# Performance work log

Measured on AMD Instinct MI355X. Metric: run time of the kernel, lower is better.

Reference implementation:

```python
import jax, jax.numpy as jnp
import numpy as np

FP8_MAX = 448.0  # finfo(float8_e4m3fn).max
G = 128          # quantization block size


def _fp8_roundtrip(x):
    # emulate storage/rounding in float8_e4m3fn
    return x.astype(jnp.float8_e4m3fn).astype(jnp.float32)


def _quant_dequant_act(x, g=G):
    """Dynamic per-token, per-128-column-group fp8 quantization, then dequant.
    Matches fp8_act_quant: scale = amax(group)/FP8_MAX, q = clip(x/scale)."""
    lead, K = x.shape[:-1], x.shape[-1]
    xg = x.reshape(*lead, K // g, g)
    amax = jnp.max(jnp.abs(xg), axis=-1, keepdims=True)
    scale = jnp.maximum(amax, 1e-10) / FP8_MAX
    q = _fp8_roundtrip(jnp.clip(xg / scale, -FP8_MAX, FP8_MAX))
    return (q * scale).reshape(*lead, K)


def _dequant_weight(w, s, g=G):
    """Block-wise dequant: w [E,O,K] fp8 codes (stored as f32), s [E,O/g,K/g] scales."""
    E, O, K = w.shape
    wb = w.reshape(E, O // g, g, K // g, g)
    return (wb * s[:, :, None, :, None]).reshape(E, O, K)


def setup_inputs() -> dict:
    key = jax.random.key(0)
    ks = jax.random.split(key, 7)
    T, H, I, E, TK = 2048, 1024, 512, 16, 4
    hidden_states = jax.random.normal(ks[0], (T, H), dtype=jnp.float32)
    top_k_index = jax.random.randint(ks[1], (T, TK), 0, E)
    top_k_weights = jax.nn.softmax(jax.random.normal(ks[2], (T, TK), dtype=jnp.float32), axis=-1)
    # fp8-representable weight codes + positive block scale grids
    gate_up_proj = _fp8_roundtrip(jax.random.normal(ks[3], (E, 2 * I, H), dtype=jnp.float32) * 8.0)
    gate_up_proj_scale_inv = jax.random.uniform(ks[4], (E, (2 * I) // G, H // G), dtype=jnp.float32,
                                                minval=0.001, maxval=0.005)
    down_proj = _fp8_roundtrip(jax.random.normal(ks[5], (E, H, I), dtype=jnp.float32) * 8.0)
    down_proj_scale_inv = jax.random.uniform(ks[6], (E, H // G, I // G), dtype=jnp.float32,
                                             minval=0.001, maxval=0.005)
    return {
        "hidden_states": hidden_states,
        "top_k_index": top_k_index,
        "top_k_weights": top_k_weights,
        "gate_up_proj": gate_up_proj,
        "gate_up_proj_scale_inv": gate_up_proj_scale_inv,
        "down_proj": down_proj,
        "down_proj_scale_inv": down_proj_scale_inv,
    }


def reference(hidden_states, top_k_index, top_k_weights,
              gate_up_proj, gate_up_proj_scale_inv,
              down_proj, down_proj_scale_inv):
    E = gate_up_proj.shape[0]
    # dynamic activation quant (identical for every expert, since tokens are just gathered rows)
    x_deq = _quant_dequant_act(hidden_states)                       # [T, H]
    w_gu = _dequant_weight(gate_up_proj, gate_up_proj_scale_inv)    # [E, 2I, H]
    w_dn = _dequant_weight(down_proj, down_proj_scale_inv)          # [E, H, I]
    # gate_up GEMM for all experts; tokens not routed to e contribute with weight 0 below
    gate_up = jnp.einsum('th,eoh->teo', x_deq, w_gu)                # [T, E, 2I]
    gate, up = jnp.split(gate_up, 2, axis=-1)
    h = jax.nn.silu(gate) * up                                      # [T, E, I]
    h_deq = _quant_dequant_act(h)                                   # re-quantize intermediate
    expert_out = jnp.einsum('tei,ehi->teh', h_deq, w_dn)            # [T, E, H]
    # routing weight per (token, expert): sum of top_k weights whose index == e
    rw = jnp.einsum('tk,tke->te', top_k_weights,
                    jax.nn.one_hot(top_k_index, E, dtype=hidden_states.dtype))
    return jnp.einsum('teh,te->th', expert_out, rw)                 # [T, H] float32 accumulation
```

## Files before the change

### kernel.cpp

```cpp
#include <hip/hip_runtime.h>
#include <math.h>

#define T_TOK 2048
#define H_DIM 1024
#define I_DIM 512
#define N_EXP 16
#define TOPK  4
#define NPAIR (T_TOK*TOPK)

typedef unsigned short u16;
typedef __attribute__((ext_vector_type(8))) short s8v;
typedef __attribute__((ext_vector_type(4))) float f4v;

#define GLDS(g, l) __builtin_amdgcn_global_load_lds( \
    (const __attribute__((address_space(1))) void*)(g), \
    (__attribute__((address_space(3))) void*)(l), 16, 0, 0)

__device__ __forceinline__ float fp8_rt(float v) {
    float av = fabsf(v);
    if (av < 0.015625f) {
        return rintf(v * 512.0f) * 0.001953125f;
    }
    unsigned u = __float_as_uint(v);
    unsigned lsb = (u >> 20) & 1u;
    u = (u + 0x7FFFFu + lsb) & 0xFFF00000u;
    return __uint_as_float(u);
}

__device__ __forceinline__ unsigned f2bf(float v) {
    return __float_as_uint(v) >> 16;
}

#define NF4_GU (N_EXP * 2 * I_DIM * H_DIM / 4)
__global__ void k_prep(const float* __restrict__ wgu, u16* __restrict__ wgu_bf,
                       const float* __restrict__ wdn, u16* __restrict__ wdn_bf,
                       const float* __restrict__ x, u16* __restrict__ xq,
                       float* __restrict__ xs, const int* __restrict__ tki,
                       int* __restrict__ counts, int* __restrict__ lists) {
    int bid = blockIdx.x, tid = threadIdx.x;
    if (bid < 24576) {
        int i = bid * 256 + tid;
        const float* in = wgu; u16* out = wgu_bf;
        if (i >= NF4_GU) { in = wdn; out = wdn_bf; i -= NF4_GU; }
        float4 a = ((const float4*)in)[i];
        int2 st;
        st.x = (int)(f2bf(a.x) | (f2bf(a.y) << 16));
        st.y = (int)(f2bf(a.z) | (f2bf(a.w) << 16));
        ((int2*)out)[i] = st;
    } else {
        int t = bid - 24576;
        if (tid < 4) {
            int p = t * 4 + tid;
            int e = tki[p];
            int pos = atomicAdd(&counts[e], 1);
            lists[e * NPAIR + pos] = p;
        }
        float4 v = ((const float4*)(x + (size_t)t * H_DIM))[tid];
        float a = fmaxf(fmaxf(fabsf(v.x), fabsf(v.y)), fmaxf(fabsf(v.z), fabsf(v.w)));
        #pragma unroll
        for (int m = 16; m >= 1; m >>= 1) a = fmaxf(a, __shfl_xor(a, m));
        float s = fmaxf(a, 1e-10f) / 448.0f;
        ushort4 r;
        r.x = (u16)f2bf(fp8_rt(fminf(fmaxf(v.x / s, -448.f), 448.f)));
        r.y = (u16)f2bf(fp8_rt(fminf(fmaxf(v.y / s, -448.f), 448.f)));
        r.z = (u16)f2bf(fp8_rt(fminf(fmaxf(v.z / s, -448.f), 448.f)));
        r.w = (u16)f2bf(fp8_rt(fminf(fmaxf(v.w / s, -448.f), 448.f)));
        ((ushort4*)(xq + (size_t)t * H_DIM))[tid] = r;
        if ((tid & 31) == 0) xs[t * 8 + (tid >> 5)] = s;
    }
}

__global__ __launch_bounds__(256, 3)
void k_gateup(const u16* __restrict__ xq, const float* __restrict__ xs,
              const int* __restrict__ counts, const int* __restrict__ lists,
              const u16* __restrict__ wgu, const float* __restrict__ sgu,
              const u16* __restrict__ zbuf, float* __restrict__ hbuf) {
    int bid = blockIdx.x;
    int e = bid & 15, tile = bid >> 4;
    int tt = tile >> 3, it = tile & 7;
    int n = counts[e];
    if (tt * 64 >= n) return;

    __shared__ __align__(16) u16 sm[2][12288];
    __shared__ float xs_l[64][8];
    __shared__ int ptok[64];

    int tid = threadIdx.x;
    int w = tid >> 6, lane = tid & 63;
    int m = w & 1, q = w >> 1;
    int l15 = lane & 15, l4 = lane >> 4;

    if (tid < 64) {
        int slot = tt * 64 + tid;
        ptok[tid] = (slot < n) ? lists[e * NPAIR + slot] : -1;
    }
    __syncthreads();
    {
        int r = tid >> 2, kb4 = (tid & 3) * 2;
        int p = ptok[r];
        xs_l[r][kb4]     = (p >= 0) ? xs[(p >> 2) * 8 + kb4]     : 0.f;
        xs_l[r][kb4 + 1] = (p >= 0) ? xs[(p >> 2) * 8 + kb4 + 1] : 0.f;
    }

    const u16* wbase = wgu + (size_t)e * 1024 * 1024;
    const u16* srcB[4];
    #pragma unroll
    for (int j = 0; j < 4; ++j) {
        int s = j * 256 + tid;
        int row = s >> 3, c = s & 7, cg = c ^ (row & 7);
        int nrow = (row < 64) ? it * 64 + row : 448 + it * 64 + row;
        srcB[j] = wbase + (size_t)nrow * H_DIM + cg * 8;
    }
    const u16* srcA[2];
    #pragma unroll
    for (int j = 0; j < 2; ++j) {
        int s = j * 256 + tid;
        int row = s >> 3, c = s & 7, cg = c ^ (row & 7);
        int p = ptok[row];
        srcA[j] = (p >= 0) ? xq + (size_t)(p >> 2) * H_DIM + cg * 8 : zbuf;
    }

    int idxA[2][2], idxB[4][2];
    #pragma unroll
    for (int fm = 0; fm < 2; ++fm) {
        int ar = m * 32 + fm * 16 + l15;
        #pragma unroll
        for (int kg = 0; kg < 2; ++kg)
            idxA[fm][kg] = 8192 + ar * 64 + (((kg * 4 + l4) ^ (ar & 7)) * 8);
    }
    #pragma unroll
    for (int nf = 0; nf < 4; ++nf) {
        int br = q * 64 + nf * 16 + l15;
        #pragma unroll
        for (int kg = 0; kg < 2; ++kg)
            idxB[nf][kg] = br * 64 + (((kg * 4 + l4) ^ (br & 7)) * 8);
    }

    auto stage = [&](int buf) {
        #pragma unroll
        for (int j = 0; j < 4; ++j) { GLDS(srcB[j], &sm[buf][j * 2048 + tid * 8]); srcB[j] += 64; }
        #pragma unroll
        for (int j = 0; j < 2; ++j) { GLDS(srcA[j], &sm[buf][8192 + j * 2048 + tid * 8]); srcA[j] += 64; }
    };

    f4v master[2][4], part[2][4];
    #pragma unroll
    for (int a = 0; a < 2; ++a)
        #pragma unroll
        for (int b = 0; b < 4; ++b) { master[a][b] = (f4v){0,0,0,0}; part[a][b] = (f4v){0,0,0,0}; }

    const float* swp = sgu + e * 64 + (q ? 4 + (it >> 1) : (it >> 1)) * 8;

    stage(0);
    __syncthreads();

    for (int t = 0; t < 16; ++t) {
        if (t < 15) stage((t + 1) & 1);
        const u16* buf = &sm[t & 1][0];
        #pragma unroll
        for (int kg = 0; kg < 2; ++kg) {
            s8v a0 = *(const s8v*)&buf[idxA[0][kg]];
            s8v a1 = *(const s8v*)&buf[idxA[1][kg]];
            #pragma unroll
            for (int nf = 0; nf < 4; ++nf) {
                s8v b = *(const s8v*)&buf[idxB[nf][kg]];
                part[0][nf] = __builtin_amdgcn_mfma_f32_16x16x32_bf16(a0, b, part[0][nf], 0, 0, 0);
                part[1][nf] = __builtin_amdgcn_mfma_f32_16x16x32_bf16(a1, b, part[1][nf], 0, 0, 0);
            }
        }
        if (t & 1) {
            int kb = t >> 1;
            float sw = swp[kb];
            #pragma unroll
            for (int fm = 0; fm < 2; ++fm) {
                float c0 = xs_l[m * 32 + fm * 16 + l4 * 4 + 0][kb] * sw;
                float c1 = xs_l[m * 32 + fm * 16 + l4 * 4 + 1][kb] * sw;
                float c2 = xs_l[m * 32 + fm * 16 + l4 * 4 + 2][kb] * sw;
                float c3 = xs_l[m * 32 + fm * 16 + l4 * 4 + 3][kb] * sw;
                #pragma unroll
                for (int nf = 0; nf < 4; ++nf) {
                    master[fm][nf][0] += c0 * part[fm][nf][0];
                    master[fm][nf][1] += c1 * part[fm][nf][1];
                    master[fm][nf][2] += c2 * part[fm][nf][2];
                    master[fm][nf][3] += c3 * part[fm][nf][3];
                    part[fm][nf] = (f4v){0,0,0,0};
                }
            }
        }
        __syncthreads();
    }

    float* Ul = (float*)sm;
    if (q == 1) {
        #pragma unroll
        for (int fm = 0; fm < 2; ++fm)
            #pragma unroll
            for (int nf = 0; nf < 4; ++nf)
                #pragma unroll
                for (int r = 0; r < 4; ++r)
                    Ul[(m * 32 + fm * 16 + l4 * 4 + r) * 65 + nf * 16 + l15] = master[fm][nf][r];
    }
    __syncthreads();
    if (q == 0) {
        #pragma unroll
        for (int fm = 0; fm < 2; ++fm)
            #pragma unroll
            for (int r = 0; r < 4; ++r) {
                int row = m * 32 + fm * 16 + l4 * 4 + r;
                int p = ptok[row];
                if (p < 0) continue;
                float* drow = hbuf + (size_t)p * I_DIM + it * 64;
                #pragma unroll
                for (int nf = 0; nf < 4; ++nf) {
                    float g = master[fm][nf][r];
                    float u = Ul[row * 65 + nf * 16 + l15];
                    drow[nf * 16 + l15] = (g / (1.0f + expf(-g))) * u;
                }
            }
    }
}

__global__ void k_quant_h(const float* __restrict__ h, u16* __restrict__ hq,
                          float* __restrict__ hs) {
    int p = blockIdx.x, tid = threadIdx.x;
    float4 v = ((const float4*)(h + (size_t)p * I_DIM))[tid];
    float a = fmaxf(fmaxf(fabsf(v.x), fabsf(v.y)), fmaxf(fabsf(v.z), fabsf(v.w)));
    #pragma unroll
    for (int m = 16; m >= 1; m >>= 1) a = fmaxf(a, __shfl_xor(a, m));
    float s = fmaxf(a, 1e-10f) / 448.0f;
    ushort4 r;
    r.x = (u16)f2bf(fp8_rt(fminf(fmaxf(v.x / s, -448.f), 448.f)));
    r.y = (u16)f2bf(fp8_rt(fminf(fmaxf(v.y / s, -448.f), 448.f)));
    r.z = (u16)f2bf(fp8_rt(fminf(fmaxf(v.z / s, -448.f), 448.f)));
    r.w = (u16)f2bf(fp8_rt(fminf(fmaxf(v.w / s, -448.f), 448.f)));
    ((ushort4*)(hq + (size_t)p * I_DIM))[tid] = r;
    if ((tid & 31) == 0) hs[p * 4 + (tid >> 5)] = s;
}

__global__ __launch_bounds__(256, 3)
void k_down(const u16* __restrict__ hq, const float* __restrict__ hs,
            const int* __restrict__ counts, const int* __restrict__ lists,
            const u16* __restrict__ wdn, const float* __restrict__ sdn,
            const float* __restrict__ tkw, const u16* __restrict__ zbuf,
            float* __restrict__ dout) {
    int bid = blockIdx.x;
    int e = bid & 15, tile = bid >> 4;
    int tt = tile >> 3, nt = tile & 7;
    int n = counts[e];
    if (tt * 64 >= n) return;

    __shared__ __align__(16) u16 sm[2][12288];
    __shared__ float hs_l[64][4];
    __shared__ float rw_l[64];
    __shared__ int ptok[64];

    int tid = threadIdx.x;
    int w = tid >> 6, lane = tid & 63;
    int m = w & 1, q = w >> 1;
    int l15 = lane & 15, l4 = lane >> 4;

    if (tid < 64) {
        int slot = tt * 64 + tid;
        ptok[tid] = (slot < n) ? lists[e * NPAIR + slot] : -1;
    }
    __syncthreads();
    {
        int r = tid >> 2, kb = tid & 3;
        int p = ptok[r];
        hs_l[r][kb] = (p >= 0) ? hs[p * 4 + kb] : 0.f;
        if (tid < 64) rw_l[tid] = (ptok[tid] >= 0) ? tkw[ptok[tid]] : 0.f;
    }

    const u16* wbase = wdn + (size_t)e * H_DIM * I_DIM;
    const u16* srcB[4];
    #pragma unroll
    for (int j = 0; j < 4; ++j) {
        int s = j * 256 + tid;
        int row = s >> 3, c = s & 7, cg = c ^ (row & 7);
        srcB[j] = wbase + (size_t)(nt * 128 + row) * I_DIM + cg * 8;
    }
    const u16* srcA[2];
    #pragma unroll
    for (int j = 0; j < 2; ++j) {
        int s = j * 256 + tid;
        int row = s >> 3, c = s & 7, cg = c ^ (row & 7);
        int p = ptok[row];
        srcA[j] = (p >= 0) ? hq + (size_t)p * I_DIM + cg * 8 : zbuf;
    }

    int idxA[2][2], idxB[4][2];
    #pragma unroll
    for (int fm = 0; fm < 2; ++fm) {
        int ar = m * 32 + fm * 16 + l15;
        #pragma unroll
        for (int kg = 0; kg < 2; ++kg)
            idxA[fm][kg] = 8192 + ar * 64 + (((kg * 4 + l4) ^ (ar & 7)) * 8);
    }
    #pragma unroll
    for (int nf = 0; nf < 4; ++nf) {
        int br = q * 64 + nf * 16 + l15;
        #pragma unroll
        for (int kg = 0; kg < 2; ++kg)
            idxB[nf][kg] = br * 64 + (((kg * 4 + l4) ^ (br & 7)) * 8);
    }

    auto stage = [&](int buf) {
        #pragma unroll
        for (int j = 0; j < 4; ++j) { GLDS(srcB[j], &sm[buf][j * 2048 + tid * 8]); srcB[j] += 64; }
        #pragma unroll
        for (int j = 0; j < 2; ++j) { GLDS(srcA[j], &sm[buf][8192 + j * 2048 + tid * 8]); srcA[j] += 64; }
    };

    f4v master[2][4], part[2][4];
    #pragma unroll
    for (int a = 0; a < 2; ++a)
        #pragma unroll
        for (int b = 0; b < 4; ++b) { master[a][b] = (f4v){0,0,0,0}; part[a][b] = (f4v){0,0,0,0}; }

    const float* swp = sdn + (e * 8 + nt) * 4;

    stage(0);
    __syncthreads();

    for (int t = 0; t < 8; ++t) {
        if (t < 7) stage((t + 1) & 1);
        const u16* buf = &sm[t & 1][0];
        #pragma unroll
        for (int kg = 0; kg < 2; ++kg) {
            s8v a0 = *(const s8v*)&buf[idxA[0][kg]];
            s8v a1 = *(const s8v*)&buf[idxA[1][kg]];
            #pragma unroll
            for (int nf = 0; nf < 4; ++nf) {
                s8v b = *(const s8v*)&buf[idxB[nf][kg]];
                part[0][nf] = __builtin_amdgcn_mfma_f32_16x16x32_bf16(a0, b, part[0][nf], 0, 0, 0);
                part[1][nf] = __builtin_amdgcn_mfma_f32_16x16x32_bf16(a1, b, part[1][nf], 0, 0, 0);
            }
        }
        if (t & 1) {
            int kb = t >> 1;
            float sw = swp[kb];
            #pragma unroll
            for (int fm = 0; fm < 2; ++fm) {
                float c0 = hs_l[m * 32 + fm * 16 + l4 * 4 + 0][kb] * sw;
                float c1 = hs_l[m * 32 + fm * 16 + l4 * 4 + 1][kb] * sw;
                float c2 = hs_l[m * 32 + fm * 16 + l4 * 4 + 2][kb] * sw;
                float c3 = hs_l[m * 32 + fm * 16 + l4 * 4 + 3][kb] * sw;
                #pragma unroll
                for (int nf = 0; nf < 4; ++nf) {
                    master[fm][nf][0] += c0 * part[fm][nf][0];
                    master[fm][nf][1] += c1 * part[fm][nf][1];
                    master[fm][nf][2] += c2 * part[fm][nf][2];
                    master[fm][nf][3] += c3 * part[fm][nf][3];
                    part[fm][nf] = (f4v){0,0,0,0};
                }
            }
        }
        __syncthreads();
    }

    #pragma unroll
    for (int fm = 0; fm < 2; ++fm)
        #pragma unroll
        for (int r = 0; r < 4; ++r) {
            int row = m * 32 + fm * 16 + l4 * 4 + r;
            int p = ptok[row];
            if (p < 0) continue;
            float rw = rw_l[row];
            float* drow = dout + (size_t)p * H_DIM + nt * 128 + q * 64;
            #pragma unroll
            for (int nf = 0; nf < 4; ++nf)
                drow[nf * 16 + l15] = rw * master[fm][nf][r];
        }
}

__global__ void k_reduce(const float* __restrict__ dout, float* __restrict__ out) {
    int i = blockIdx.x * 256 + threadIdx.x;
    int t = i >> 8, h4 = i & 255;
    const float4* d = (const float4*)dout;
    float4 a = d[(size_t)(t * 4 + 0) * 256 + h4];
    float4 b = d[(size_t)(t * 4 + 1) * 256 + h4];
    float4 c = d[(size_t)(t * 4 + 2) * 256 + h4];
    float4 e = d[(size_t)(t * 4 + 3) * 256 + h4];
    float4 r;
    r.x = a.x + b.x + c.x + e.x;
    r.y = a.y + b.y + c.y + e.y;
    r.z = a.z + b.z + c.z + e.z;
    r.w = a.w + b.w + c.w + e.w;
    ((float4*)out)[i] = r;
}

extern "C" void kernel_launch(void* const* d_in, const int* in_sizes, int n_in,
                              void* d_out, int out_size, void* d_ws, size_t ws_size,
                              hipStream_t stream) {
    const float* hs_in = (const float*)d_in[0];
    const int*   tki = (const int*)d_in[1];
    const float* tkw = (const float*)d_in[2];
    const float* wgu = (const float*)d_in[3];
    const float* sgu = (const float*)d_in[4];
    const float* wdn = (const float*)d_in[5];
    const float* sdn = (const float*)d_in[6];
    float* out = (float*)d_out;

    char* ws = (char*)d_ws;
    const size_t MB = 1024 * 1024;
    u16*   wgu_bf = (u16*)(ws);
    float* dout   = (float*)(ws);
    u16*   wdn_bf = (u16*)(ws + 32 * MB);
    u16*   xq     = (u16*)(ws + 48 * MB);
    float* xs     = (float*)(ws + 52 * MB);
    float* hbuf   = (float*)(ws + 53 * MB);
    u16*   hq     = (u16*)(ws + 69 * MB);
    float* hs     = (float*)(ws + 77 * MB);
    int*   counts = (int*)(ws + 78 * MB);
    u16*   zbuf   = (u16*)(ws + 78 * MB + 4096);
    int*   lists  = (int*)(ws + 78 * MB + 65536);

    hipMemsetAsync(ws + 78 * MB, 0, 8192, stream);

    k_prep<<<26624, 256, 0, stream>>>(wgu, wgu_bf, wdn, wdn_bf, hs_in, xq, xs,
                                      tki, counts, lists);
    k_gateup<<<2048, 256, 0, stream>>>(xq, xs, counts, lists, wgu_bf, sgu, zbuf, hbuf);
    k_quant_h<<<NPAIR, 128, 0, stream>>>(hbuf, hq, hs);
    k_down<<<2048, 256, 0, stream>>>(hq, hs, counts, lists, wdn_bf, sdn, tkw, zbuf, dout);
    k_reduce<<<T_TOK * H_DIM / 1024, 256, 0, stream>>>(dout, out);
}
```

Measured before the change: 249.6 us.

## Switch expert GEMMs from bf16 to native fp8 MFMA with byte-packed operands

Weights and quantized activations are now stored as packed fp8 e4m3 bytes instead of bf16, and both expert GEMMs use the fp8 MFMA instruction. This halves the bytes written by the prep kernel and the bytes streamed into LDS by the GEMMs, and halves the K-loop trip count since each 128-byte row holds a full 128-element scale block. The block scale is now applied every iteration instead of every other one. Routing is moved into a separate single-block kernel that counts with LDS atomics, which adds one launch and a serial 8192-pair pass. The handwritten fp8 encoder must match the hardware e4m3 format, including denormals.

```diff
diff --git a/kernel.cpp b/kernel.cpp
--- a/kernel.cpp
+++ b/kernel.cpp
@@ -9,7 +9,7 @@
 #define NPAIR (T_TOK*TOPK)
 
 typedef unsigned short u16;
-typedef __attribute__((ext_vector_type(8))) short s8v;
+typedef unsigned char u8;
 typedef __attribute__((ext_vector_type(4))) float f4v;
 
 #define GLDS(g, l) __builtin_amdgcn_global_load_lds( \
@@ -27,61 +27,73 @@
     return __uint_as_float(u);
 }
 
-__device__ __forceinline__ unsigned f2bf(float v) {
-    return __float_as_uint(v) >> 16;
+__device__ __forceinline__ unsigned f2fp8(float v) {
+    unsigned u = __float_as_uint(v);
+    unsigned s = (u >> 24) & 0x80u;
+    float av = fabsf(v);
+    if (av < 0.015625f) return s | (unsigned)(av * 512.0f);
+    unsigned e = ((u >> 23) & 0xFFu) - 120u;
+    return s | (e << 3) | ((u >> 20) & 7u);
+}
+
+__global__ void k_route2(const int* __restrict__ tki, int* __restrict__ counts,
+                         int* __restrict__ lists) {
+    __shared__ int cnt[16];
+    int tid = threadIdx.x;
+    if (tid < 16) cnt[tid] = 0;
+    __syncthreads();
+    #pragma unroll
+    for (int j = 0; j < 8; ++j) {
+        int p = tid * 8 + j;
+        int e = tki[p];
+        int pos = atomicAdd(&cnt[e], 1);
+        lists[e * NPAIR + pos] = p;
+    }
+    __syncthreads();
+    if (tid < 16) counts[tid] = cnt[tid];
 }
 
 #define NF4_GU (N_EXP * 2 * I_DIM * H_DIM / 4)
-__global__ void k_prep(const float* __restrict__ wgu, u16* __restrict__ wgu_bf,
-                       const float* __restrict__ wdn, u16* __restrict__ wdn_bf,
-                       const float* __restrict__ x, u16* __restrict__ xq,
-                       float* __restrict__ xs, const int* __restrict__ tki,
-                       int* __restrict__ counts, int* __restrict__ lists) {
+__global__ void k_prep(const float* __restrict__ wgu, u8* __restrict__ wgu_f8,
+                       const float* __restrict__ wdn, u8* __restrict__ wdn_f8,
+                       const float* __restrict__ x, u8* __restrict__ xq,
+                       float* __restrict__ xs) {
     int bid = blockIdx.x, tid = threadIdx.x;
     if (bid < 24576) {
         int i = bid * 256 + tid;
-        const float* in = wgu; u16* out = wgu_bf;
-        if (i >= NF4_GU) { in = wdn; out = wdn_bf; i -= NF4_GU; }
+        const float* in = wgu; u8* out = wgu_f8;
+        if (i >= NF4_GU) { in = wdn; out = wdn_f8; i -= NF4_GU; }
         float4 a = ((const float4*)in)[i];
-        int2 st;
-        st.x = (int)(f2bf(a.x) | (f2bf(a.y) << 16));
-        st.y = (int)(f2bf(a.z) | (f2bf(a.w) << 16));
-        ((int2*)out)[i] = st;
+        unsigned pk = f2fp8(a.x) | (f2fp8(a.y) << 8) | (f2fp8(a.z) << 16) | (f2fp8(a.w) << 24);
+        ((unsigned*)out)[i] = pk;
     } else {
         int t = bid - 24576;
-        if (tid < 4) {
-            int p = t * 4 + tid;
-            int e = tki[p];
-            int pos = atomicAdd(&counts[e], 1);
-            lists[e * NPAIR + pos] = p;
-        }
         float4 v = ((const float4*)(x + (size_t)t * H_DIM))[tid];
         float a = fmaxf(fmaxf(fabsf(v.x), fabsf(v.y)), fmaxf(fabsf(v.z), fabsf(v.w)));
         #pragma unroll
         for (int m = 16; m >= 1; m >>= 1) a = fmaxf(a, __shfl_xor(a, m));
         float s = fmaxf(a, 1e-10f) / 448.0f;
-        ushort4 r;
-        r.x = (u16)f2bf(fp8_rt(fminf(fmaxf(v.x / s, -448.f), 448.f)));
-        r.y = (u16)f2bf(fp8_rt(fminf(fmaxf(v.y / s, -448.f), 448.f)));
-        r.z = (u16)f2bf(fp8_rt(fminf(fmaxf(v.z / s, -448.f), 448.f)));
-        r.w = (u16)f2bf(fp8_rt(fminf(fmaxf(v.w / s, -448.f), 448.f)));
-        ((ushort4*)(xq + (size_t)t * H_DIM))[tid] = r;
+        unsigned pk = f2fp8(fp8_rt(fminf(fmaxf(v.x / s, -448.f), 448.f)))
+                    | (f2fp8(fp8_rt(fminf(fmaxf(v.y / s, -448.f), 448.f))) << 8)
+                    | (f2fp8(fp8_rt(fminf(fmaxf(v.z / s, -448.f), 448.f))) << 16)
+                    | (f2fp8(fp8_rt(fminf(fmaxf(v.w / s, -448.f), 448.f))) << 24);
+        ((unsigned*)(xq + (size_t)t * H_DIM))[tid] = pk;
         if ((tid & 31) == 0) xs[t * 8 + (tid >> 5)] = s;
     }
 }
 
 __global__ __launch_bounds__(256, 3)
-void k_gateup(const u16* __restrict__ xq, const float* __restrict__ xs,
+void k_gateup(const u8* __restrict__ xq, const float* __restrict__ xs,
               const int* __restrict__ counts, const int* __restrict__ lists,
-              const u16* __restrict__ wgu, const float* __restrict__ sgu,
-              const u16* __restrict__ zbuf, float* __restrict__ hbuf) {
+              const u8* __restrict__ wgu, const float* __restrict__ sgu,
+              const u8* __restrict__ zbuf, float* __restrict__ hbuf) {
     int bid = blockIdx.x;
     int e = bid & 15, tile = bid >> 4;
     int tt = tile >> 3, it = tile & 7;
     int n = counts[e];
     if (tt * 64 >= n) return;
 
-    __shared__ __align__(16) u16 sm[2][12288];
+    __shared__ __align__(16) u8 sm[2][24576];
     __shared__ float xs_l[64][8];
     __shared__ int ptok[64];
 
@@ -102,45 +114,49 @@
         xs_l[r][kb4 + 1] = (p >= 0) ? xs[(p >> 2) * 8 + kb4 + 1] : 0.f;
     }
 
-    const u16* wbase = wgu + (size_t)e * 1024 * 1024;
-    const u16* srcB[4];
+    const u8* wbase = wgu + (size_t)e * (2 * I_DIM) * H_DIM;
+    const u8* srcB[4];
     #pragma unroll
     for (int j = 0; j < 4; ++j) {
         int s = j * 256 + tid;
-        int row = s >> 3, c = s & 7, cg = c ^ (row & 7);
+        int row = s >> 3, c8 = s & 7, cg = c8 ^ (row & 7);
         int nrow = (row < 64) ? it * 64 + row : 448 + it * 64 + row;
-        srcB[j] = wbase + (size_t)nrow * H_DIM + cg * 8;
-    }
-    const u16* srcA[2];
+        srcB[j] = wbase + (size_t)nrow * H_DIM + cg * 16;
+    }
+    const u8* srcA[2];
     #pragma unroll
     for (int j = 0; j < 2; ++j) {
         int s = j * 256 + tid;
-        int row = s >> 3, c = s & 7, cg = c ^ (row & 7);
+        int row = s >> 3, c8 = s & 7, cg = c8 ^ (row & 7);
         int p = ptok[row];
-        srcA[j] = (p >= 0) ? xq + (size_t)(p >> 2) * H_DIM + cg * 8 : zbuf;
-    }
-
-    int idxA[2][2], idxB[4][2];
+        srcA[j] = (p >= 0) ? xq + (size_t)(p >> 2) * H_DIM + cg * 16 : zbuf;
+    }
+
+    int idxA[2][4], idxB[4][4];
     #pragma unroll
     for (int fm = 0; fm < 2; ++fm) {
         int ar = m * 32 + fm * 16 + l15;
         #pragma unroll
-        for (int kg = 0; kg < 2; ++kg)
-            idxA[fm][kg] = 8192 + ar * 64 + (((kg * 4 + l4) ^ (ar & 7)) * 8);
+        for (int kg = 0; kg < 4; ++kg) {
+            int u = kg * 4 + l4;
+            idxA[fm][kg] = 16384 + ar * 128 + (((u >> 1) ^ (ar & 7)) << 4) + ((u & 1) << 3);
+        }
     }
     #pragma unroll
     for (int nf = 0; nf < 4; ++nf) {
         int br = q * 64 + nf * 16 + l15;
         #pragma unroll
-        for (int kg = 0; kg < 2; ++kg)
-            idxB[nf][kg] = br * 64 + (((kg * 4 + l4) ^ (br & 7)) * 8);
+        for (int kg = 0; kg < 4; ++kg) {
+            int u = kg * 4 + l4;
+            idxB[nf][kg] = br * 128 + (((u >> 1) ^ (br & 7)) << 4) + ((u & 1) << 3);
+        }
     }
 
     auto stage = [&](int buf) {
         #pragma unroll
-        for (int j = 0; j < 4; ++j) { GLDS(srcB[j], &sm[buf][j * 2048 + tid * 8]); srcB[j] += 64; }
-        #pragma unroll
-        for (int j = 0; j < 2; ++j) { GLDS(srcA[j], &sm[buf][8192 + j * 2048 + tid * 8]); srcA[j] += 64; }
+        for (int j = 0; j < 4; ++j) { GLDS(srcB[j], &sm[buf][(j * 256 + tid) * 16]); srcB[j] += 128; }
+        #pragma unroll
+        for (int j = 0; j < 2; ++j) { GLDS(srcA[j], &sm[buf][16384 + (j * 256 + tid) * 16]); srcA[j] += 128; }
     };
 
     f4v master[2][4], part[2][4];
@@ -154,29 +170,28 @@
     stage(0);
     __syncthreads();
 
-    for (int t = 0; t < 16; ++t) {
-        if (t < 15) stage((t + 1) & 1);
-        const u16* buf = &sm[t & 1][0];
-        #pragma unroll
-        for (int kg = 0; kg < 2; ++kg) {
-            s8v a0 = *(const s8v*)&buf[idxA[0][kg]];
-            s8v a1 = *(const s8v*)&buf[idxA[1][kg]];
+    for (int t = 0; t < 8; ++t) {
+        if (t < 7) stage((t + 1) & 1);
+        const u8* buf = &sm[t & 1][0];
+        #pragma unroll
+        for (int kg = 0; kg < 4; ++kg) {
+            long a0 = *(const long*)&buf[idxA[0][kg]];
+            long a1 = *(const long*)&buf[idxA[1][kg]];
             #pragma unroll
             for (int nf = 0; nf < 4; ++nf) {
-                s8v b = *(const s8v*)&buf[idxB[nf][kg]];
-                part[0][nf] = __builtin_amdgcn_mfma_f32_16x16x32_bf16(a0, b, part[0][nf], 0, 0, 0);
-                part[1][nf] = __builtin_amdgcn_mfma_f32_16x16x32_bf16(a1, b, part[1][nf], 0, 0, 0);
+                long b = *(const long*)&buf[idxB[nf][kg]];
+                part[0][nf] = __builtin_amdgcn_mfma_f32_16x16x32_fp8_fp8(a0, b, part[0][nf], 0, 0, 0);
+                part[1][nf] = __builtin_amdgcn_mfma_f32_16x16x32_fp8_fp8(a1, b, part[1][nf], 0, 0, 0);
             }
         }
-        if (t & 1) {
-            int kb = t >> 1;
-            float sw = swp[kb];
+        {
+            float sw = swp[t];
             #pragma unroll
             for (int fm = 0; fm < 2; ++fm) {
-                float c0 = xs_l[m * 32 + fm * 16 + l4 * 4 + 0][kb] * sw;
-                float c1 = xs_l[m * 32 + fm * 16 + l4 * 4 + 1][kb] * sw;
-                float c2 = xs_l[m * 32 + fm * 16 + l4 * 4 + 2][kb] * sw;
-                float c3 = xs_l[m * 32 + fm * 16 + l4 * 4 + 3][kb] * sw;
+                float c0 = xs_l[m * 32 + fm * 16 + l4 * 4 + 0][t] * sw;
+                float c1 = xs_l[m * 32 + fm * 16 + l4 * 4 + 1][t] * sw;
+                float c2 = xs_l[m * 32 + fm * 16 + l4 * 4 + 2][t] * sw;
+                float c3 = xs_l[m * 32 + fm * 16 + l4 * 4 + 3][t] * sw;
                 #pragma unroll
                 for (int nf = 0; nf < 4; ++nf) {
                     master[fm][nf][0] += c0 * part[fm][nf][0];
@@ -220,7 +235,7 @@
     }
 }
 
-__global__ void k_quant_h(const float* __restrict__ h, u16* __restrict__ hq,
+__global__ void k_quant_h(const float* __restrict__ h, u8* __restrict__ hq,
                           float* __restrict__ hs) {
     int p = blockIdx.x, tid = threadIdx.x;
     float4 v = ((const float4*)(h + (size_t)p * I_DIM))[tid];
@@ -228,20 +243,19 @@
     #pragma unroll
     for (int m = 16; m >= 1; m >>= 1) a = fmaxf(a, __shfl_xor(a, m));
     float s = fmaxf(a, 1e-10f) / 448.0f;
-    ushort4 r;
-    r.x = (u16)f2bf(fp8_rt(fminf(fmaxf(v.x / s, -448.f), 448.f)));
-    r.y = (u16)f2bf(fp8_rt(fminf(fmaxf(v.y / s, -448.f), 448.f)));
-    r.z = (u16)f2bf(fp8_rt(fminf(fmaxf(v.z / s, -448.f), 448.f)));
-    r.w = (u16)f2bf(fp8_rt(fminf(fmaxf(v.w / s, -448.f), 448.f)));
-    ((ushort4*)(hq + (size_t)p * I_DIM))[tid] = r;
+    unsigned pk = f2fp8(fp8_rt(fminf(fmaxf(v.x / s, -448.f), 448.f)))
+                | (f2fp8(fp8_rt(fminf(fmaxf(v.y / s, -448.f), 448.f))) << 8)
+                | (f2fp8(fp8_rt(fminf(fmaxf(v.z / s, -448.f), 448.f))) << 16)
+                | (f2fp8(fp8_rt(fminf(fmaxf(v.w / s, -448.f), 448.f))) << 24);
+    ((unsigned*)(hq + (size_t)p * I_DIM))[tid] = pk;
     if ((tid & 31) == 0) hs[p * 4 + (tid >> 5)] = s;
 }
 
 __global__ __launch_bounds__(256, 3)
-void k_down(const u16* __restrict__ hq, const float* __restrict__ hs,
+void k_down(const u8* __restrict__ hq, const float* __restrict__ hs,
             const int* __restrict__ counts, const int* __restrict__ lists,
-            const u16* __restrict__ wdn, const float* __restrict__ sdn,
-            const float* __restrict__ tkw, const u16* __restrict__ zbuf,
+            const u8* __restrict__ wdn, const float* __restrict__ sdn,
+            const float* __restrict__ tkw, const u8* __restrict__ zbuf,
             float* __restrict__ dout) {
     int bid = blockIdx.x;
     int e = bid & 15, tile = bid >> 4;
@@ -249,7 +263,7 @@
     int n = counts[e];
     if (tt * 64 >= n) return;
 
-    __shared__ __align__(16) u16 sm[2][12288];
+    __shared__ __align__(16) u8 sm[2][24576];
     __shared__ float hs_l[64][4];
     __shared__ float rw_l[64];
     __shared__ int ptok[64];
@@ -271,44 +285,48 @@
         if (tid < 64) rw_l[tid] = (ptok[tid] >= 0) ? tkw[ptok[tid]] : 0.f;
     }
 
-    const u16* wbase = wdn + (size_t)e * H_DIM * I_DIM;
-    const u16* srcB[4];
+    const u8* wbase = wdn + (size_t)e * H_DIM * I_DIM;
+    const u8* srcB[4];
     #pragma unroll
     for (int j = 0; j < 4; ++j) {
         int s = j * 256 + tid;
-        int row = s >> 3, c = s & 7, cg = c ^ (row & 7);
-        srcB[j] = wbase + (size_t)(nt * 128 + row) * I_DIM + cg * 8;
-    }
-    const u16* srcA[2];
+        int row = s >> 3, c8 = s & 7, cg = c8 ^ (row & 7);
+        srcB[j] = wbase + (size_t)(nt * 128 + row) * I_DIM + cg * 16;
+    }
+    const u8* srcA[2];
     #pragma unroll
     for (int j = 0; j < 2; ++j) {
         int s = j * 256 + tid;
-        int row = s >> 3, c = s & 7, cg = c ^ (row & 7);
+        int row = s >> 3, c8 = s & 7, cg = c8 ^ (row & 7);
         int p = ptok[row];
-        srcA[j] = (p >= 0) ? hq + (size_t)p * I_DIM + cg * 8 : zbuf;
-    }
-
-    int idxA[2][2], idxB[4][2];
+        srcA[j] = (p >= 0) ? hq + (size_t)p * I_DIM + cg * 16 : zbuf;
+    }
+
+    int idxA[2][4], idxB[4][4];
     #pragma unroll
     for (int fm = 0; fm < 2; ++fm) {
         int ar = m * 32 + fm * 16 + l15;
         #pragma unroll
-        for (int kg = 0; kg < 2; ++kg)
-            idxA[fm][kg] = 8192 + ar * 64 + (((kg * 4 + l4) ^ (ar & 7)) * 8);
+        for (int kg = 0; kg < 4; ++kg) {
+            int u = kg * 4 + l4;
+            idxA[fm][kg] = 16384 + ar * 128 + (((u >> 1) ^ (ar & 7)) << 4) + ((u & 1) << 3);
+        }
     }
     #pragma unroll
     for (int nf = 0; nf < 4; ++nf) {
         int br = q * 64 + nf * 16 + l15;
         #pragma unroll
-        for (int kg = 0; kg < 2; ++kg)
-            idxB[nf][kg] = br * 64 + (((kg * 4 + l4) ^ (br & 7)) * 8);
+        for (int kg = 0; kg < 4; ++kg) {
+            int u = kg * 4 + l4;
+            idxB[nf][kg] = br * 128 + (((u >> 1) ^ (br & 7)) << 4) + ((u & 1) << 3);
+        }
     }
 
     auto stage = [&](int buf) {
         #pragma unroll
-        for (int j = 0; j < 4; ++j) { GLDS(srcB[j], &sm[buf][j * 2048 + tid * 8]); srcB[j] += 64; }
-        #pragma unroll
-        for (int j = 0; j < 2; ++j) { GLDS(srcA[j], &sm[buf][8192 + j * 2048 + tid * 8]); srcA[j] += 64; }
+        for (int j = 0; j < 4; ++j) { GLDS(srcB[j], &sm[buf][(j * 256 + tid) * 16]); srcB[j] += 128; }
+        #pragma unroll
+        for (int j = 0; j < 2; ++j) { GLDS(srcA[j], &sm[buf][16384 + (j * 256 + tid) * 16]); srcA[j] += 128; }
     };
 
     f4v master[2][4], part[2][4];
@@ -322,29 +340,28 @@
     stage(0);
     __syncthreads();
 
-    for (int t = 0; t < 8; ++t) {
-        if (t < 7) stage((t + 1) & 1);
-        const u16* buf = &sm[t & 1][0];
-        #pragma unroll
-        for (int kg = 0; kg < 2; ++kg) {
-            s8v a0 = *(const s8v*)&buf[idxA[0][kg]];
-            s8v a1 = *(const s8v*)&buf[idxA[1][kg]];
+    for (int t = 0; t < 4; ++t) {
+        if (t < 3) stage((t + 1) & 1);
+        const u8* buf = &sm[t & 1][0];
+        #pragma unroll
+        for (int kg = 0; kg < 4; ++kg) {
+            long a0 = *(const long*)&buf[idxA[0][kg]];
+            long a1 = *(const long*)&buf[idxA[1][kg]];
             #pragma unroll
             for (int nf = 0; nf < 4; ++nf) {
-                s8v b = *(const s8v*)&buf[idxB[nf][kg]];
-                part[0][nf] = __builtin_amdgcn_mfma_f32_16x16x32_bf16(a0, b, part[0][nf], 0, 0, 0);
-                part[1][nf] = __builtin_amdgcn_mfma_f32_16x16x32_bf16(a1, b, part[1][nf], 0, 0, 0);
+                long b = *(const long*)&buf[idxB[nf][kg]];
+                part[0][nf] = __builtin_amdgcn_mfma_f32_16x16x32_fp8_fp8(a0, b, part[0][nf], 0, 0, 0);
+                part[1][nf] = __builtin_amdgcn_mfma_f32_16x16x32_fp8_fp8(a1, b, part[1][nf], 0, 0, 0);
             }
         }
-        if (t & 1) {
-            int kb = t >> 1;
-            float sw = swp[kb];
+        {
+            float sw = swp[t];
             #pragma unroll
             for (int fm = 0; fm < 2; ++fm) {
-                float c0 = hs_l[m * 32 + fm * 16 + l4 * 4 + 0][kb] * sw;
-                float c1 = hs_l[m * 32 + fm * 16 + l4 * 4 + 1][kb] * sw;
-                float c2 = hs_l[m * 32 + fm * 16 + l4 * 4 + 2][kb] * sw;
-                float c3 = hs_l[m * 32 + fm * 16 + l4 * 4 + 3][kb] * sw;
+                float c0 = hs_l[m * 32 + fm * 16 + l4 * 4 + 0][t] * sw;
+                float c1 = hs_l[m * 32 + fm * 16 + l4 * 4 + 1][t] * sw;
+                float c2 = hs_l[m * 32 + fm * 16 + l4 * 4 + 2][t] * sw;
+                float c3 = hs_l[m * 32 + fm * 16 + l4 * 4 + 3][t] * sw;
                 #pragma unroll
                 for (int nf = 0; nf < 4; ++nf) {
                     master[fm][nf][0] += c0 * part[fm][nf][0];
@@ -403,24 +420,24 @@
 
     char* ws = (char*)d_ws;
     const size_t MB = 1024 * 1024;
-    u16*   wgu_bf = (u16*)(ws);
+    u8*    wgu_f8 = (u8*)(ws);
     float* dout   = (float*)(ws);
-    u16*   wdn_bf = (u16*)(ws + 32 * MB);
-    u16*   xq     = (u16*)(ws + 48 * MB);
-    float* xs     = (float*)(ws + 52 * MB);
-    float* hbuf   = (float*)(ws + 53 * MB);
-    u16*   hq     = (u16*)(ws + 69 * MB);
-    float* hs     = (float*)(ws + 77 * MB);
-    int*   counts = (int*)(ws + 78 * MB);
-    u16*   zbuf   = (u16*)(ws + 78 * MB + 4096);
-    int*   lists  = (int*)(ws + 78 * MB + 65536);
-
-    hipMemsetAsync(ws + 78 * MB, 0, 8192, stream);
-
-    k_prep<<<26624, 256, 0, stream>>>(wgu, wgu_bf, wdn, wdn_bf, hs_in, xq, xs,
-                                      tki, counts, lists);
-    k_gateup<<<2048, 256, 0, stream>>>(xq, xs, counts, lists, wgu_bf, sgu, zbuf, hbuf);
+    u8*    wdn_f8 = (u8*)(ws + 32 * MB);
+    u8*    xq     = (u8*)(ws + 40 * MB);
+    float* xs     = (float*)(ws + 42 * MB);
+    float* hbuf   = (float*)(ws + 43 * MB);
+    u8*    hq     = (u8*)(ws + 59 * MB);
+    float* hs     = (float*)(ws + 63 * MB);
+    int*   counts = (int*)(ws + 64 * MB);
+    u8*    zbuf   = (u8*)(ws + 64 * MB + 4096);
+    int*   lists  = (int*)(ws + 64 * MB + 65536);
+
+    hipMemsetAsync(ws + 64 * MB, 0, 8192, stream);
+
+    k_route2<<<1, 1024, 0, stream>>>(tki, counts, lists);
+    k_prep<<<26624, 256, 0, stream>>>(wgu, wgu_f8, wdn, wdn_f8, hs_in, xq, xs);
+    k_gateup<<<2048, 256, 0, stream>>>(xq, xs, counts, lists, wgu_f8, sgu, zbuf, hbuf);
     k_quant_h<<<NPAIR, 128, 0, stream>>>(hbuf, hq, hs);
-    k_down<<<2048, 256, 0, stream>>>(hq, hs, counts, lists, wdn_bf, sdn, tkw, zbuf, dout);
+    k_down<<<2048, 256, 0, stream>>>(hq, hs, counts, lists, wdn_f8, sdn, tkw, zbuf, dout);
     k_reduce<<<T_TOK * H_DIM / 1024, 256, 0, stream>>>(dout, out);
 }
```

After: 214.1 us. 14.2% less time.
